# Kernel tuning notes

Hardware: AMD Instinct MI355X
Metric: run time of the kernel (lower is better)

## Reference

```python
import jax, jax.numpy as jnp
import numpy as np

B, S, D = 4, 2048, 2048
H, HD = 16, 128
MAX_SEQ = 2048


def setup_inputs() -> dict:
    key = jax.random.key(0)
    ks = jax.random.split(key, 6)
    scale = 1.0 / np.sqrt(D)
    h = jax.random.normal(ks[0], (B, S, D), dtype=jnp.float32)
    Wq = jax.random.normal(ks[1], (D, H * HD), dtype=jnp.float32) * scale
    Wk = jax.random.normal(ks[2], (D, H * HD), dtype=jnp.float32) * scale
    Wv = jax.random.normal(ks[3], (D, H * HD), dtype=jnp.float32) * scale
    Wo = jax.random.normal(ks[4], (H * HD, D), dtype=jnp.float32) * scale
    # torch Linear stores weight as [out, in]; keep that layout
    Wq, Wk, Wv, Wo = Wq.T, Wk.T, Wv.T, Wo.T
    K_cache = jnp.zeros((B, H, MAX_SEQ, HD), dtype=jnp.float32)
    V_cache = jnp.zeros((B, H, MAX_SEQ, HD), dtype=jnp.float32)
    # standard RoPE angles: theta = pos / 10000^(2i/hd)
    inv_freq = 1.0 / (10000.0 ** (np.arange(0, HD, 2, dtype=np.float32) / HD))
    t = np.arange(MAX_SEQ, dtype=np.float32)
    ang = np.outer(t, inv_freq)  # [MAX_SEQ, HD//2]
    freqs_cos = jnp.asarray(np.cos(ang), dtype=jnp.float32)
    freqs_sin = jnp.asarray(np.sin(ang), dtype=jnp.float32)
    return {"h": h, "Wq": Wq, "Wk": Wk, "Wv": Wv, "Wo": Wo,
            "K_cache": K_cache, "V_cache": V_cache,
            "freqs_cos": freqs_cos, "freqs_sin": freqs_sin, "pos": 0}


def _rope(x, cos, sin):
    # x: [B,H,S,HD]; cos/sin: [1,1,S,HD//2]; complex multiply on (even,odd) pairs
    xr = x.reshape(*x.shape[:-1], -1, 2)
    x0, x1 = xr[..., 0], xr[..., 1]
    out = jnp.stack([x0 * cos - x1 * sin, x0 * sin + x1 * cos], axis=-1)
    return out.reshape(x.shape)


def reference(h, Wq, Wk, Wv, Wo, K_cache, V_cache, freqs_cos, freqs_sin, pos):
    Bq, Sq, _ = h.shape
    Q = jnp.einsum('bsd,ed->bse', h, Wq).reshape(Bq, Sq, H, HD).transpose(0, 2, 1, 3)
    K = jnp.einsum('bsd,ed->bse', h, Wk).reshape(Bq, Sq, H, HD).transpose(0, 2, 1, 3)
    V = jnp.einsum('bsd,ed->bse', h, Wv).reshape(Bq, Sq, H, HD).transpose(0, 2, 1, 3)
    cos = freqs_cos[pos:pos + Sq][None, None]
    sin = freqs_sin[pos:pos + Sq][None, None]
    Q = _rope(Q, cos, sin)
    K = _rope(K, cos, sin)
    # KV-cache append then read back prefix
    K_full = jax.lax.dynamic_update_slice(K_cache, K, (0, 0, pos, 0))
    V_full = jax.lax.dynamic_update_slice(V_cache, V, (0, 0, pos, 0))
    L = pos + Sq
    K_all = K_full[:, :, :L]
    V_all = V_full[:, :, :L]
    scores = jnp.einsum('bhqd,bhkd->bhqk', Q, K_all) / jnp.sqrt(jnp.float32(HD))
    if Sq > 1:  # causal: query at absolute position pos+i attends keys <= pos+i
        mask = (pos + jnp.arange(Sq))[:, None] >= jnp.arange(L)[None, :]
        scores = jnp.where(mask[None, None], scores, jnp.float32(-1e30))
    attn = jax.nn.softmax(scores, axis=-1)
    out = jnp.einsum('bhqk,bhkd->bhqd', attn, V_all)
    out = out.transpose(0, 2, 1, 3).reshape(Bq, Sq, H * HD)
    return jnp.einsum('bse,de->bsd', out, Wo)
```

## Files before the change

kernel.cpp:

```cpp
#include <hip/hip_runtime.h>
#include <hip/hip_bf16.h>

typedef __attribute__((ext_vector_type(8))) short bf16x8;
typedef __attribute__((ext_vector_type(4))) float f32x4;
typedef __attribute__((ext_vector_type(4))) unsigned short u16x4;

#define BB 4
#define SS 2048
#define DD 2048
#define HH 16
#define HDD 128
#define MASKV (-30000.0f)
#define MINIT (-15000.0f)

__device__ __forceinline__ unsigned short f2bf(float f) {
  __hip_bfloat16 b = __float2bfloat16(f);
  return *reinterpret_cast<unsigned short*>(&b);
}
__device__ __forceinline__ void gl_lds16(const void* g, void* l) {
  __builtin_amdgcn_global_load_lds((const __attribute__((address_space(1))) unsigned int*)g,
                                   (__attribute__((address_space(3))) unsigned int*)l, 16, 0, 0);
}

__global__ __launch_bounds__(256) void convertk(const float* __restrict__ src,
                                                __hip_bfloat16* __restrict__ dst, int n4) {
  int i = blockIdx.x * 256 + threadIdx.x;
  if (i >= n4) return;
  f32x4 v = ((const f32x4*)src)[i];
  u16x4 o;
  o[0] = f2bf(v[0]); o[1] = f2bf(v[1]); o[2] = f2bf(v[2]); o[3] = f2bf(v[3]);
  ((u16x4*)dst)[i] = o;
}

template <int MODE>
__global__ __launch_bounds__(512, 1) void gemm256(const __hip_bfloat16* __restrict__ A,
                                                  const __hip_bfloat16* __restrict__ Bw,
                                                  __hip_bfloat16* __restrict__ Cbf,
                                                  __hip_bfloat16* __restrict__ Vt,
                                                  float* __restrict__ Cf,
                                                  const float* __restrict__ fc,
                                                  const float* __restrict__ fs,
                                                  const int* __restrict__ posp,
                                                  int M, int N, int K) {
  __shared__ __hip_bfloat16 As[4][256 * 32];
  __shared__ __hip_bfloat16 Bs[4][256 * 32];
  const int tid = threadIdx.x;
  const int wid = tid >> 6, lane = tid & 63;
  const int l15 = lane & 15, l4 = lane >> 4;
  const int wm = wid >> 2, wn = wid & 3;

  const int nbn = N >> 8;
  const int nb = (M >> 8) * nbn;
  const int bid = blockIdx.x;
  const int swz = (bid & 7) * (nb >> 3) + (bid >> 3);
  const int bm = swz / nbn, bn = swz % nbn;

  const int NT = K >> 5;

#define STAGE_TILE(TT, BUF)                                                       \
  {                                                                               \
    const int k0_ = (TT) << 5;                                                    \
    _Pragma("unroll") for (int i = 0; i < 2; i++) {                               \
      int c = i * 512 + tid, rr = c >> 2, jj = (c & 3) ^ ((rr >> 1) & 3);         \
      gl_lds16(A + ((long)bm * 256 + rr) * K + k0_ + jj * 8,                      \
               &As[BUF][0] + c * 8);                                              \
      gl_lds16(Bw + ((long)bn * 256 + rr) * K + k0_ + jj * 8,                     \
               &Bs[BUF][0] + c * 8);                                              \
    }                                                                             \
  }

  f32x4 acc[8][4] = {};

  STAGE_TILE(0, 0);
  STAGE_TILE(1, 1);

  for (int T = 0; T < NT; ++T) {
    const int cb = T & 3;
    if (T + 2 < NT) STAGE_TILE(T + 2, (T + 2) & 3);

    if (T + 2 < NT)      asm volatile("s_waitcnt vmcnt(8)" ::: "memory");
    else if (T + 1 < NT) asm volatile("s_waitcnt vmcnt(4)" ::: "memory");
    else                 asm volatile("s_waitcnt vmcnt(0)" ::: "memory");
    __builtin_amdgcn_s_barrier();
    asm volatile("" ::: "memory");

    bf16x8 af[8], bg[4];
#pragma unroll
    for (int ni = 0; ni < 4; ni++) {
      int r = wn * 64 + ni * 16 + l15;
      int j = l4 ^ ((r >> 1) & 3);
      bg[ni] = *(const bf16x8*)(&Bs[cb][0] + r * 32 + j * 8);
    }
#pragma unroll
    for (int mi = 0; mi < 8; mi++) {
      int r = wm * 128 + mi * 16 + l15;
      int j = l4 ^ ((r >> 1) & 3);
      af[mi] = *(const bf16x8*)(&As[cb][0] + r * 32 + j * 8);
    }
    __builtin_amdgcn_s_setprio(1);
#pragma unroll
    for (int mi = 0; mi < 8; mi++)
#pragma unroll
      for (int ni = 0; ni < 4; ni++)
        acc[mi][ni] = __builtin_amdgcn_mfma_f32_16x16x32_bf16(af[mi], bg[ni],
                                                              acc[mi][ni], 0, 0, 0);
    __builtin_amdgcn_s_setprio(0);
  }
#undef STAGE_TILE

  if (MODE == 0) {
    if (bn * 256 < 4096) {
      const int pos = *posp;
#pragma unroll
      for (int mi = 0; mi < 8; mi++)
#pragma unroll
        for (int ni = 0; ni < 4; ni++) {
          int n = bn * 256 + wn * 64 + ni * 16 + l15;
          int hd = n & 127;
          int ip = hd >> 1;
          bool odd = hd & 1;
#pragma unroll
          for (int r = 0; r < 4; r++) {
            float v = acc[mi][ni][r];
            float p = __shfl_xor(v, 1, 64);
            int m = bm * 256 + wm * 128 + mi * 16 + l4 * 4 + r;
            int s = m & (SS - 1);
            float cv = fc[(long)(pos + s) * 64 + ip];
            float sv = fs[(long)(pos + s) * 64 + ip];
            float out = odd ? (p * sv + v * cv) : (v * cv - p * sv);
            Cbf[(long)m * 4096 + n] = __float2bfloat16(out);
          }
        }
    } else {
#pragma unroll
      for (int mi = 0; mi < 8; mi++)
#pragma unroll
        for (int ni = 0; ni < 4; ni++) {
          int e = bn * 256 + wn * 64 + ni * 16 + l15 - 4096;
          int hh = e >> 7, hd = e & 127;
          int m0 = bm * 256 + wm * 128 + mi * 16 + l4 * 4;
          int b = m0 >> 11, s0 = m0 & (SS - 1);
          u16x4 pk;
#pragma unroll
          for (int r = 0; r < 4; r++) pk[r] = f2bf(acc[mi][ni][r]);
          *(u16x4*)(Vt + (((long)(b * HH + hh) * 128 + hd) * SS + s0)) = pk;
        }
    }
  } else {
#pragma unroll
    for (int mi = 0; mi < 8; mi++)
#pragma unroll
      for (int ni = 0; ni < 4; ni++) {
        int n = bn * 256 + wn * 64 + ni * 16 + l15;
#pragma unroll
        for (int r = 0; r < 4; r++) {
          int m = bm * 256 + wm * 128 + mi * 16 + l4 * 4 + r;
          Cf[(long)m * N + n] = acc[mi][ni][r];
        }
      }
  }
}

__global__ __launch_bounds__(256, 2) void attn_k(const __hip_bfloat16* __restrict__ qk,
                                                 const __hip_bfloat16* __restrict__ vt,
                                                 __hip_bfloat16* __restrict__ aout,
                                                 const int* __restrict__ posp) {
  __shared__ __hip_bfloat16 Ks[64 * 128];
  __shared__ __hip_bfloat16 Vs[128 * 64];
  __shared__ __hip_bfloat16 Ps[4][16 * 64];
  const int pos = *posp;
  const int orig = blockIdx.x;
  const int swz = (orig & 7) * 128 + (orig >> 3);
  const int qp = swz & 15, bh = swz >> 4;
  const int b = bh >> 4, h = bh & 15;
  const int tid = threadIdx.x;
  const int wave = tid >> 6, lane = tid & 63;
  const int l15 = lane & 15, l4 = lane >> 4;

  const long kbase = ((long)b * SS) * 4096 + 2048 + h * 128;
  const long vbase = ((long)bh * 128) * SS;
  const float sc2 = 0.08838834764831845f * 1.4426950408889634f;

  const int s_kr[4] = {(0 * 256 + tid) >> 4, (1 * 256 + tid) >> 4, (2 * 256 + tid) >> 4, (3 * 256 + tid) >> 4};
  const int s_kc = tid & 15;
  const int s_hd[4] = {(0 * 256 + tid) >> 3, (1 * 256 + tid) >> 3, (2 * 256 + tid) >> 3, (3 * 256 + tid) >> 3};
  const int s_vc = tid & 7;

  bf16x8 kreg[4], vreg[4];

#define LOADKV(T)                                                                             \
  {                                                                                           \
    const int kv0_ = (T) * 64;                                                                \
    _Pragma("unroll") for (int i = 0; i < 4; i++) {                                           \
      kreg[i] = *(const bf16x8*)(qk + kbase + (long)(kv0_ + s_kr[i]) * 4096 + s_kc * 8);      \
      vreg[i] = *(const bf16x8*)(vt + vbase + (long)s_hd[i] * SS + kv0_ + s_vc * 8);          \
    }                                                                                         \
  }

#define STAGE()                                                                               \
  {                                                                                           \
    _Pragma("unroll") for (int i = 0; i < 4; i++) {                                           \
      *(bf16x8*)(Ks + ((s_kr[i] * 128 + s_kc * 8) ^ ((s_kr[i] & 7) << 3))) = kreg[i];         \
      *(bf16x8*)(Vs + ((s_hd[i] * 64 + s_vc * 8) ^ ((s_hd[i] & 7) << 3))) = vreg[i];          \
    }                                                                                         \
  }

  for (int half = 0; half < 2; ++half) {
    const int qb = half ? (31 - qp) : qp;
    const int qwb = qb * 64 + wave * 16;

    bf16x8 qf[4];
#pragma unroll
    for (int kk = 0; kk < 4; kk++) {
      long row = (long)b * SS + qwb + l15;
      qf[kk] = *(const bf16x8*)(qk + row * 4096 + h * 128 + kk * 32 + l4 * 8);
    }

    f32x4 accO[8] = {};
    float mrun[4], lrun[4];
#pragma unroll
    for (int r = 0; r < 4; r++) { mrun[r] = MINIT; lrun[r] = 0.f; }

    int ntiles = (pos + qb * 64 + 63) / 64 + 1;
    if (ntiles > SS / 64) ntiles = SS / 64;
#define TT(t) (half ? (ntiles - 1 - (t)) : (t))

    LOADKV(TT(0));
    __syncthreads();
    STAGE();

    for (int t = 0; t < ntiles; ++t) {
      const int kv0 = TT(t) * 64;
      __syncthreads();
      if (t + 1 < ntiles) LOADKV(TT(t + 1));

      f32x4 sfr[4] = {};
      __builtin_amdgcn_s_setprio(1);
#pragma unroll
      for (int ni = 0; ni < 4; ni++) {
        const int key = ni * 16 + l15;
        const int sw = (key & 7) << 3;
#pragma unroll
        for (int kk = 0; kk < 4; kk++) {
          bf16x8 kf = *(const bf16x8*)(Ks + ((key * 128 + kk * 32 + l4 * 8) ^ sw));
          sfr[ni] = __builtin_amdgcn_mfma_f32_16x16x32_bf16(qf[kk], kf, sfr[ni], 0, 0, 0);
        }
      }
      __builtin_amdgcn_s_setprio(0);

      const bool needmask = (kv0 + 63) > (pos + qb * 64);
#pragma unroll
      for (int ni = 0; ni < 4; ni++)
#pragma unroll
        for (int r = 0; r < 4; r++) {
          float v = sfr[ni][r] * sc2;
          if (needmask) {
            int key = kv0 + ni * 16 + l15;
            int q = qwb + l4 * 4 + r;
            if (key > pos + q) v = MASKV;
          }
          sfr[ni][r] = v;
        }

      {
        f32x4 mx = sfr[0];
#pragma unroll
        for (int ni = 1; ni < 4; ni++)
#pragma unroll
          for (int r = 0; r < 4; r++) mx[r] = fmaxf(mx[r], sfr[ni][r]);
#pragma unroll
        for (int d = 1; d < 16; d <<= 1)
#pragma unroll
          for (int r = 0; r < 4; r++) mx[r] = fmaxf(mx[r], __shfl_xor(mx[r], d, 64));

        float growth = mx[0] - mrun[0];
#pragma unroll
        for (int r = 1; r < 4; r++) growth = fmaxf(growth, mx[r] - mrun[r]);
        if (!__all(growth <= 11.0f)) {
          float scal[4];
#pragma unroll
          for (int r = 0; r < 4; r++) {
            float mn = fmaxf(mrun[r], mx[r]);
            scal[r] = exp2f(mrun[r] - mn);
            mrun[r] = mn;
            lrun[r] *= scal[r];
          }
#pragma unroll
          for (int ni = 0; ni < 8; ni++)
#pragma unroll
            for (int r = 0; r < 4; r++) accO[ni][r] *= scal[r];
        }

        f32x4 rs = {0.f, 0.f, 0.f, 0.f};
#pragma unroll
        for (int ni = 0; ni < 4; ni++)
#pragma unroll
          for (int r = 0; r < 4; r++) {
            float p = exp2f(sfr[ni][r] - mrun[r]);
            rs[r] += p;
            int prow = l4 * 4 + r;
            Ps[wave][(prow * 64 + ni * 16 + l15) ^ ((prow & 7) << 3)] = __float2bfloat16(p);
          }
#pragma unroll
        for (int d = 1; d < 16; d <<= 1)
#pragma unroll
          for (int r = 0; r < 4; r++) rs[r] += __shfl_xor(rs[r], d, 64);
#pragma unroll
        for (int r = 0; r < 4; r++) lrun[r] += rs[r];
      }

      __builtin_amdgcn_s_setprio(1);
#pragma unroll
      for (int kk = 0; kk < 2; kk++) {
        int prow = l15;
        bf16x8 pf = *(const bf16x8*)(Ps[wave] + ((prow * 64 + kk * 32 + l4 * 8) ^ ((prow & 7) << 3)));
#pragma unroll
        for (int ni = 0; ni < 8; ni++) {
          int hd = ni * 16 + l15;
          bf16x8 vf = *(const bf16x8*)(Vs + ((hd * 64 + kk * 32 + l4 * 8) ^ ((hd & 7) << 3)));
          accO[ni] = __builtin_amdgcn_mfma_f32_16x16x32_bf16(pf, vf, accO[ni], 0, 0, 0);
        }
      }
      __builtin_amdgcn_s_setprio(0);

      __syncthreads();
      if (t + 1 < ntiles) STAGE();
    }
#undef TT

    __hip_bfloat16* E = Ks + wave * 2048;
    {
      float inv[4];
#pragma unroll
      for (int r = 0; r < 4; r++) inv[r] = 1.0f / lrun[r];
#pragma unroll
      for (int ni = 0; ni < 8; ni++)
#pragma unroll
        for (int r = 0; r < 4; r++) {
          int row = l4 * 4 + r;
          E[(row * 128 + ni * 16 + l15) ^ ((row & 7) << 3)] =
              __float2bfloat16(accO[ni][r] * inv[r]);
        }
    }
    const long gb = ((long)b * SS + qwb) * 2048 + h * 128;
#pragma unroll
    for (int j = 0; j < 4; j++) {
      int row = j * 4 + l4;
      int c8 = l15 * 8;
      bf16x8 v = *(const bf16x8*)(E + ((row * 128 + c8) ^ ((row & 7) << 3)));
      *(bf16x8*)(aout + gb + (long)row * 2048 + c8) = v;
    }
  }
#undef LOADKV
#undef STAGE
}

extern "C" void kernel_launch(void* const* d_in, const int* in_sizes, int n_in,
                              void* d_out, int out_size, void* d_ws, size_t ws_size,
                              hipStream_t stream) {
  (void)in_sizes; (void)n_in; (void)out_size; (void)ws_size;
  const float* h  = (const float*)d_in[0];
  const float* Wq = (const float*)d_in[1];
  const float* Wk = (const float*)d_in[2];
  const float* Wv = (const float*)d_in[3];
  const float* Wo = (const float*)d_in[4];
  const float* fc = (const float*)d_in[7];
  const float* fs = (const float*)d_in[8];
  const int* pos  = (const int*)d_in[9];
  float* out = (float*)d_out;

  char* ws = (char*)d_ws;
  __hip_bfloat16* hb    = (__hip_bfloat16*)(ws);
  __hip_bfloat16* wqkv  = (__hip_bfloat16*)(ws + 33554432);
  __hip_bfloat16* wo_b  = (__hip_bfloat16*)(ws + 58720256);
  __hip_bfloat16* qkbuf = (__hip_bfloat16*)(ws + 67108864);
  __hip_bfloat16* vt    = (__hip_bfloat16*)(ws + 134217728);
  __hip_bfloat16* aout  = hb;

  convertk<<<16384, 256, 0, stream>>>(h, hb, 4194304);
  convertk<<<4096, 256, 0, stream>>>(Wq, wqkv, 1048576);
  convertk<<<4096, 256, 0, stream>>>(Wk, wqkv + 4194304, 1048576);
  convertk<<<4096, 256, 0, stream>>>(Wv, wqkv + 8388608, 1048576);
  convertk<<<4096, 256, 0, stream>>>(Wo, wo_b, 1048576);

  gemm256<0><<<768, 512, 0, stream>>>(hb, wqkv, qkbuf, vt, nullptr, fc, fs, pos,
                                      8192, 6144, 2048);

  attn_k<<<1024, 256, 0, stream>>>(qkbuf, vt, aout, pos);

  gemm256<1><<<256, 512, 0, stream>>>(aout, wo_b, nullptr, nullptr, out, nullptr,
                                      nullptr, nullptr, 8192, 2048, 2048);
}
```

Before: 505.0 us.

## Deepen GEMM prefetch to three tiles and split loads across half-iterations

The GEMM main loop now prefetches three K-tiles ahead instead of two, using all four LDS buffers. It splits each iteration into two halves separated by a barrier, issuing the A-tile global-to-LDS loads in the first half and the B-tile loads in the second, with the MFMA work divided to match. The goal is to hide more global load latency and spread load issue across the compute. The cost is an extra barrier per iteration, and the vmcnt accounting now relies on the split issue order being correct.

```diff
diff --git a/kernel.cpp b/kernel.cpp
--- a/kernel.cpp
+++ b/kernel.cpp
@@ -57,34 +57,41 @@
 
   const int NT = K >> 5;
 
-#define STAGE_TILE(TT, BUF)                                                       \
+#define STAGE_A(TT, BUF)                                                          \
   {                                                                               \
     const int k0_ = (TT) << 5;                                                    \
     _Pragma("unroll") for (int i = 0; i < 2; i++) {                               \
       int c = i * 512 + tid, rr = c >> 2, jj = (c & 3) ^ ((rr >> 1) & 3);         \
-      gl_lds16(A + ((long)bm * 256 + rr) * K + k0_ + jj * 8,                      \
-               &As[BUF][0] + c * 8);                                              \
-      gl_lds16(Bw + ((long)bn * 256 + rr) * K + k0_ + jj * 8,                     \
-               &Bs[BUF][0] + c * 8);                                              \
+      gl_lds16(A + ((long)bm * 256 + rr) * K + k0_ + jj * 8, &As[BUF][0] + c * 8);\
     }                                                                             \
   }
+#define STAGE_B(TT, BUF)                                                          \
+  {                                                                               \
+    const int k0_ = (TT) << 5;                                                    \
+    _Pragma("unroll") for (int i = 0; i < 2; i++) {                               \
+      int c = i * 512 + tid, rr = c >> 2, jj = (c & 3) ^ ((rr >> 1) & 3);         \
+      gl_lds16(Bw + ((long)bn * 256 + rr) * K + k0_ + jj * 8, &Bs[BUF][0] + c * 8);\
+    }                                                                             \
+  }
 
   f32x4 acc[8][4] = {};
 
-  STAGE_TILE(0, 0);
-  STAGE_TILE(1, 1);
+  STAGE_A(0, 0); STAGE_B(0, 0);
+  STAGE_A(1, 1); STAGE_B(1, 1);
+  STAGE_A(2, 2); STAGE_B(2, 2);
 
   for (int T = 0; T < NT; ++T) {
     const int cb = T & 3;
-    if (T + 2 < NT) STAGE_TILE(T + 2, (T + 2) & 3);
-
-    if (T + 2 < NT)      asm volatile("s_waitcnt vmcnt(8)" ::: "memory");
-    else if (T + 1 < NT) asm volatile("s_waitcnt vmcnt(4)" ::: "memory");
-    else                 asm volatile("s_waitcnt vmcnt(0)" ::: "memory");
+    const int rem = NT - 1 - T;
+
+    if (rem >= 2)      asm volatile("s_waitcnt vmcnt(8)" ::: "memory");
+    else if (rem == 1) asm volatile("s_waitcnt vmcnt(4)" ::: "memory");
+    else               asm volatile("s_waitcnt vmcnt(0)" ::: "memory");
     __builtin_amdgcn_s_barrier();
     asm volatile("" ::: "memory");
 
-    bf16x8 af[8], bg[4];
+    if (T + 3 < NT) STAGE_A(T + 3, (T + 3) & 3);
+    bf16x8 bg[4], af0[4];
 #pragma unroll
     for (int ni = 0; ni < 4; ni++) {
       int r = wn * 64 + ni * 16 + l15;
@@ -92,21 +99,41 @@
       bg[ni] = *(const bf16x8*)(&Bs[cb][0] + r * 32 + j * 8);
     }
 #pragma unroll
-    for (int mi = 0; mi < 8; mi++) {
+    for (int mi = 0; mi < 4; mi++) {
       int r = wm * 128 + mi * 16 + l15;
       int j = l4 ^ ((r >> 1) & 3);
-      af[mi] = *(const bf16x8*)(&As[cb][0] + r * 32 + j * 8);
+      af0[mi] = *(const bf16x8*)(&As[cb][0] + r * 32 + j * 8);
     }
     __builtin_amdgcn_s_setprio(1);
 #pragma unroll
-    for (int mi = 0; mi < 8; mi++)
+    for (int mi = 0; mi < 4; mi++)
 #pragma unroll
       for (int ni = 0; ni < 4; ni++)
-        acc[mi][ni] = __builtin_amdgcn_mfma_f32_16x16x32_bf16(af[mi], bg[ni],
+        acc[mi][ni] = __builtin_amdgcn_mfma_f32_16x16x32_bf16(af0[mi], bg[ni],
                                                               acc[mi][ni], 0, 0, 0);
     __builtin_amdgcn_s_setprio(0);
-  }
-#undef STAGE_TILE
+    __builtin_amdgcn_s_barrier();
+    asm volatile("" ::: "memory");
+
+    if (T + 3 < NT) STAGE_B(T + 3, (T + 3) & 3);
+    bf16x8 af1[4];
+#pragma unroll
+    for (int mi = 0; mi < 4; mi++) {
+      int r = wm * 128 + (mi + 4) * 16 + l15;
+      int j = l4 ^ ((r >> 1) & 3);
+      af1[mi] = *(const bf16x8*)(&As[cb][0] + r * 32 + j * 8);
+    }
+    __builtin_amdgcn_s_setprio(1);
+#pragma unroll
+    for (int mi = 0; mi < 4; mi++)
+#pragma unroll
+      for (int ni = 0; ni < 4; ni++)
+        acc[mi + 4][ni] = __builtin_amdgcn_mfma_f32_16x16x32_bf16(af1[mi], bg[ni],
+                                                                  acc[mi + 4][ni], 0, 0, 0);
+    __builtin_amdgcn_s_setprio(0);
+  }
+#undef STAGE_A
+#undef STAGE_B
 
   if (MODE == 0) {
     if (bn * 256 < 4096) {
```

Result: slower. 612.3 us (+21.2%).
